# Optimization experiments

Measured on AMD Instinct MI355X. Metric: run time of the kernel, lower is better.

The kernel has to match this reference:

```python
import jax, jax.numpy as jnp
import numpy as np

Q_SIZE = 1024
K_SIZE = 1024
NUM_UNITS = 1024
B, T_Q, T_K = 16, 64, 128


def setup_inputs() -> dict:
    key = jax.random.key(0)
    k1, k2, k3, k4, k5 = jax.random.split(key, 5)
    stdv = 1.0 / np.sqrt(NUM_UNITS)
    query = jax.random.normal(k1, (B, T_Q, Q_SIZE), dtype=jnp.float32)
    keys = jax.random.normal(k2, (B, T_K, K_SIZE), dtype=jnp.float32)
    # nn.Linear(in, out, bias=False) weight has shape (out, in)
    Wq = jax.random.uniform(k3, (NUM_UNITS, Q_SIZE), dtype=jnp.float32,
                            minval=-stdv, maxval=stdv)
    Wk = jax.random.uniform(k4, (NUM_UNITS, K_SIZE), dtype=jnp.float32,
                            minval=-stdv, maxval=stdv)
    linear_att = jax.random.uniform(k5, (NUM_UNITS,), dtype=jnp.float32,
                                    minval=-stdv, maxval=stdv)
    normalize_scalar = jnp.full((1,), stdv, dtype=jnp.float32)
    normalize_bias = jnp.zeros((NUM_UNITS,), dtype=jnp.float32)
    return {"query": query, "keys": keys, "Wq": Wq, "Wk": Wk,
            "linear_att": linear_att, "normalize_scalar": normalize_scalar,
            "normalize_bias": normalize_bias}


def reference(query, keys, Wq, Wk, linear_att, normalize_scalar, normalize_bias):
    # batch_first=True, 3-d query, math='fp32', normalize=True, dropout=0, no mask
    att_query = jnp.einsum('bqi,ni->bqn', query, Wq)   # (b, t_q, n)
    att_keys = jnp.einsum('bki,ni->bkn', keys, Wk)     # (b, t_k, n)
    # broadcast sum + bias: (b, t_q, t_k, n)
    sum_qk = att_query[:, :, None, :] + att_keys[:, None, :, :] + normalize_bias
    la = linear_att / jnp.linalg.norm(linear_att)
    la = la * normalize_scalar  # (n,) via broadcast with (1,)
    scores = jnp.einsum('bqkn,n->bqk', jnp.tanh(sum_qk), la)  # (b, t_q, t_k)
    scores_normalized = jax.nn.softmax(scores, axis=-1)
    context = jnp.einsum('bqk,bkn->bqn', scores_normalized, keys)
    return context, scores_normalized
```

## Files before the change

kernel.cpp:

```cpp
#include <hip/hip_runtime.h>
#include <hip/hip_bf16.h>
#include <math.h>


#define ALPHA_2LOG2E 2.8853900817779268f
#define LOG2E 1.4426950408889634f

typedef __attribute__((ext_vector_type(8))) short short8;
typedef __attribute__((ext_vector_type(4))) float f32x4;
typedef __attribute__((ext_vector_type(2))) float f32x2;

static __device__ __forceinline__ short f2bf(float f) {
    union { float f; unsigned u; } v; v.f = f;
    unsigned r = v.u + 0x7fffu + ((v.u >> 16) & 1u);
    return (short)(r >> 16);
}

__global__ __launch_bounds__(256) void cast_prep_kernel(
    const float* __restrict__ q, const float* __restrict__ k,
    const float* __restrict__ wq, const float* __restrict__ wk,
    short* __restrict__ qb, short* __restrict__ kb,
    short* __restrict__ wqb, short* __restrict__ wkb,
    const float* __restrict__ la, const float* __restrict__ scal,
    float* __restrict__ la2, float* __restrict__ sla)
{
    const int bid = blockIdx.x;
    if (bid == 2560) {
        __shared__ float red[4];
        const int t = threadIdx.x, lane = t & 63, w = t >> 6;
        float ss = 0.f;
        for (int i = t; i < 1024; i += 256) { float v = la[i]; ss = fmaf(v, v, ss); }
        #pragma unroll
        for (int off = 32; off; off >>= 1) ss += __shfl_xor(ss, off, 64);
        if (lane == 0) red[w] = ss;
        __syncthreads();
        const float tot = red[0] + red[1] + red[2] + red[3];
        const float sc = scal[0] / sqrtf(tot);
        float s2 = 0.f;
        for (int i = t; i < 1024; i += 256) {
            float v = la[i] * sc;
            la2[i] = 2.f * v;
            s2 += v;
        }
        #pragma unroll
        for (int off = 32; off; off >>= 1) s2 += __shfl_xor(s2, off, 64);
        __syncthreads();
        if (lane == 0) red[w] = s2;
        __syncthreads();
        if (t == 0) sla[0] = red[0] + red[1] + red[2] + red[3];
        return;
    }
    const float* src; short* dst; int base;
    if (bid < 512)       { src = q;  dst = qb;  base = bid; }
    else if (bid < 1536) { src = k;  dst = kb;  base = bid - 512; }
    else if (bid < 2048) { src = wq; dst = wqb; base = bid - 1536; }
    else                 { src = wk; dst = wkb; base = bid - 2048; }
    const size_t i = ((size_t)base * 256 + threadIdx.x) * 8;
    float4 a = *reinterpret_cast<const float4*>(src + i);
    float4 b = *reinterpret_cast<const float4*>(src + i + 4);
    short8 o;
    o[0] = f2bf(a.x); o[1] = f2bf(a.y); o[2] = f2bf(a.z); o[3] = f2bf(a.w);
    o[4] = f2bf(b.x); o[5] = f2bf(b.y); o[6] = f2bf(b.z); o[7] = f2bf(b.w);
    *reinterpret_cast<short8*>(dst + i) = o;
}

__global__ __launch_bounds__(256) void gemm_mfma_kernel(
    const short* __restrict__ qb, const short* __restrict__ kb,
    const short* __restrict__ wqb, const short* __restrict__ wkb,
    const float* __restrict__ bias,
    float* __restrict__ aqE, float* __restrict__ akE)
{
    __shared__ short As[2][64][32];
    __shared__ short Bs[2][64][32];

    const int bid = blockIdx.x;
    const short* A; const short* W; float* C; int useBias, bm, bn, ldc;
    if (bid < 256) {
        A = qb;  W = wqb; C = aqE; useBias = 0; ldc = 1024;
        bm = (bid & 15) * 64; bn = (bid >> 4) * 64;
    } else {
        int b2 = bid - 256;
        A = wkb; W = kb;  C = akE; useBias = 1; ldc = 2048;
        bm = (b2 & 15) * 64; bn = (b2 >> 4) * 64;
    }

    const int t = threadIdx.x;
    const int lane = t & 63, wid = t >> 6;
    const int wr = wid >> 1, wc = wid & 1;
    const int fr = lane & 15, fg = lane >> 4;

    const int sRow = t >> 2, sSlot = t & 3;
    const short8* pA = (const short8*)(A + (size_t)bm * 1024);
    const short8* pB = (const short8*)(W + (size_t)bn * 1024);

    const f32x4 zero = {0.f, 0.f, 0.f, 0.f};
    f32x4 acc[2][2];
    acc[0][0] = zero; acc[0][1] = zero; acc[1][0] = zero; acc[1][1] = zero;

    short8 rA = pA[(size_t)sRow * 128 + sSlot];
    short8 rB = pB[(size_t)sRow * 128 + sSlot];
    *(short8*)&As[0][sRow][sSlot * 8] = rA;
    *(short8*)&Bs[0][sRow][sSlot * 8] = rB;
    rA = pA[(size_t)sRow * 128 + 4 + sSlot];
    rB = pB[(size_t)sRow * 128 + 4 + sSlot];
    asm volatile("s_waitcnt lgkmcnt(0)" ::: "memory");
    __builtin_amdgcn_s_barrier();
    asm volatile("" ::: "memory");

    #pragma unroll 1
    for (int kt = 0; kt < 32; ++kt) {
        const int cur = kt & 1;
        short8 af[2], bfr[2];
        #pragma unroll
        for (int mi = 0; mi < 2; ++mi)
            af[mi] = *(const short8*)&As[cur][wr * 32 + mi * 16 + fr][fg * 8];
        #pragma unroll
        for (int ni = 0; ni < 2; ++ni)
            bfr[ni] = *(const short8*)&Bs[cur][wc * 32 + ni * 16 + fr][fg * 8];
        if (kt < 31) {
            *(short8*)&As[cur ^ 1][sRow][sSlot * 8] = rA;
            *(short8*)&Bs[cur ^ 1][sRow][sSlot * 8] = rB;
        }
        if (kt < 30) {
            const int koff = (kt + 2) * 4 + sSlot;
            rA = pA[(size_t)sRow * 128 + koff];
            rB = pB[(size_t)sRow * 128 + koff];
        }
        #pragma unroll
        for (int mi = 0; mi < 2; ++mi)
            #pragma unroll
            for (int ni = 0; ni < 2; ++ni)
                acc[mi][ni] = __builtin_amdgcn_mfma_f32_16x16x32_bf16(
                    af[mi], bfr[ni], acc[mi][ni], 0, 0, 0);
        asm volatile("s_waitcnt lgkmcnt(0)" ::: "memory");
        __builtin_amdgcn_s_barrier();
        asm volatile("" ::: "memory");
    }

    float* Cb = C + (size_t)bm * ldc;
    #pragma unroll
    for (int mi = 0; mi < 2; ++mi) {
        const int row0 = wr * 32 + mi * 16 + fg * 4;
        float brow[4] = {0.f, 0.f, 0.f, 0.f};
        if (useBias) {
            #pragma unroll
            for (int r = 0; r < 4; ++r) brow[r] = bias[bm + row0 + r];
        }
        #pragma unroll
        for (int ni = 0; ni < 2; ++ni) {
            const int col = bn + wc * 32 + ni * 16 + fr;
            #pragma unroll
            for (int r = 0; r < 4; ++r)
                Cb[(size_t)(row0 + r) * ldc + col] =
                    __builtin_amdgcn_exp2f((acc[mi][ni][r] + brow[r]) * ALPHA_2LOG2E);
        }
    }
}

__global__ __launch_bounds__(1024) void scores_part_kernel(
    const float* __restrict__ aqE, const float* __restrict__ akE,
    const float* __restrict__ la2, float* __restrict__ partials)
{
    const int b = blockIdx.x, nc = blockIdx.y;
    const int t = threadIdx.x, w = t >> 6, lane = t & 63;

    __shared__ float eqs[64][64];
    __shared__ float eks[64][128];
    __shared__ float l2s[64];

    {
        const int qq = t >> 4, nj = (t & 15) << 2;
        *(float4*)&eqs[qq][nj] =
            *(const float4*)(aqE + ((size_t)((b << 6) + qq) << 10) + (nc << 6) + nj);
        const int n = t >> 4, k0 = (t & 15) << 3;
        const float* src = akE + ((size_t)((nc << 6) + n) << 11) + (b << 7) + k0;
        *(float4*)&eks[n][k0]     = *(const float4*)src;
        *(float4*)&eks[n][k0 + 4] = *(const float4*)(src + 4);
        if (t < 64) l2s[t] = la2[(nc << 6) + t];
    }
    __syncthreads();

    const int q0 = w << 2;
    f32x2 acc[4];
    #pragma unroll
    for (int i = 0; i < 4; ++i) acc[i] = (f32x2){0.f, 0.f};

    const int kb2 = lane << 1;
    #pragma unroll 4
    for (int np = 0; np < 32; ++np) {
        const int n0 = np << 1;
        const f32x2 ek0 = *(const f32x2*)&eks[n0][kb2];
        const f32x2 ek1 = *(const f32x2*)&eks[n0 + 1][kb2];
        const f32x2 l2 = *(const f32x2*)&l2s[n0];
        const float S = l2.x + l2.y;
        #pragma unroll
        for (int i = 0; i < 4; ++i) {
            const f32x2 eq = *(const f32x2*)&eqs[q0 + i][n0];
            const f32x2 E0 = eq.x * ek0;
            const f32x2 E1 = eq.y * ek1;
            const f32x2 d1 = E1 + 1.f;
            const f32x2 D  = E0 * d1 + d1;
            const f32x2 num = l2.x * E1 + (l2.y * E0 + S);
            f32x2 r;
            r.x = __builtin_amdgcn_rcpf(D.x);
            r.y = __builtin_amdgcn_rcpf(D.y);
            acc[i] = num * r + acc[i];
        }
    }

    float* pp = partials + ((size_t)((b << 4) + nc) << 13) + kb2;
    #pragma unroll
    for (int i = 0; i < 4; ++i)
        *(f32x2*)(pp + ((q0 + i) << 7)) = acc[i];
}

__global__ __launch_bounds__(256) void reduce_softmax_kernel(
    const float* __restrict__ partials, const float* __restrict__ sla,
    float* __restrict__ p_buf, float* __restrict__ out_scores)
{
    const int b = blockIdx.x, qo = blockIdx.y;
    const int t = threadIdx.x, w = t >> 6, lane = t & 63;
    const int q = (qo << 2) + w;

    const float* pp = partials + ((size_t)b << 17) + (q << 7) + (lane << 1);
    float s0 = 0.f, s1 = 0.f;
    #pragma unroll
    for (int nc = 0; nc < 16; ++nc) {
        const float2 v = *(const float2*)(pp + ((size_t)nc << 13));
        s0 += v.x; s1 += v.y;
    }
    const float Sla = sla[0];
    s0 = Sla - s0; s1 = Sla - s1;
    float m = fmaxf(s0, s1);
    #pragma unroll
    for (int off = 32; off; off >>= 1) m = fmaxf(m, __shfl_xor(m, off, 64));
    float e0 = __builtin_amdgcn_exp2f((s0 - m) * LOG2E);
    float e1 = __builtin_amdgcn_exp2f((s1 - m) * LOG2E);
    float s = e0 + e1;
    #pragma unroll
    for (int off = 32; off; off >>= 1) s += __shfl_xor(s, off, 64);
    const float inv = __builtin_amdgcn_rcpf(s);
    float2 p = {e0 * inv, e1 * inv};
    *(float2*)(p_buf + ((size_t)((b << 6) + q) << 7) + (lane << 1)) = p;
    *(float2*)(out_scores + ((size_t)((b << 6) + q) << 7) + (lane << 1)) = p;
}

__global__ __launch_bounds__(512) void ctx_kernel(
    const float* __restrict__ p_buf, const float* __restrict__ keys,
    float* __restrict__ ctx)
{
    const int b = blockIdx.x, nc = blockIdx.y;
    const int t = threadIdx.x;

    __shared__ float ks[128][64];
    __shared__ float ps[64][128];

    {
        const int k = t >> 2, n0 = (t & 3) << 4;
        const float* src = keys + ((size_t)((b << 7) + k) << 10) + (nc << 6) + n0;
        #pragma unroll
        for (int i = 0; i < 4; ++i)
            *(float4*)&ks[k][n0 + (i << 2)] = *(const float4*)(src + (i << 2));
        const int qq = t >> 3, k0 = (t & 7) << 4;
        const float* psrc = p_buf + ((size_t)((b << 6) + qq) << 7) + k0;
        #pragma unroll
        for (int i = 0; i < 4; ++i)
            *(float4*)&ps[qq][k0 + (i << 2)] = *(const float4*)(psrc + (i << 2));
    }
    __syncthreads();

    const int q0 = (t >> 5) << 2;
    const int n0 = (t & 31) << 1;
    float acc[4][2];
    #pragma unroll
    for (int i = 0; i < 4; ++i) { acc[i][0] = 0.f; acc[i][1] = 0.f; }

    #pragma unroll 8
    for (int k = 0; k < 128; ++k) {
        const float2 kv = *(const float2*)&ks[k][n0];
        #pragma unroll
        for (int i = 0; i < 4; ++i) {
            const float p = ps[q0 + i][k];
            acc[i][0] = fmaf(p, kv.x, acc[i][0]);
            acc[i][1] = fmaf(p, kv.y, acc[i][1]);
        }
    }
    #pragma unroll
    for (int i = 0; i < 4; ++i) {
        float2 v = {acc[i][0], acc[i][1]};
        *(float2*)(ctx + ((size_t)((b << 6) + q0 + i) << 10) + (nc << 6) + n0) = v;
    }
}

extern "C" void kernel_launch(void* const* d_in, const int* in_sizes, int n_in,
                              void* d_out, int out_size, void* d_ws, size_t ws_size,
                              hipStream_t stream) {
    const float* query  = (const float*)d_in[0];
    const float* keys   = (const float*)d_in[1];
    const float* Wq     = (const float*)d_in[2];
    const float* Wk     = (const float*)d_in[3];
    const float* la     = (const float*)d_in[4];
    const float* scal   = (const float*)d_in[5];
    const float* bias   = (const float*)d_in[6];

    float* ws  = (float*)d_ws;
    float* aqE = ws;
    float* akE = ws + (1u << 20);
    float* la2 = akE + (2u << 20);
    float* sla = la2 + 1024;
    short* qb  = (short*)(ws + 3 * 1048576 + 2048);
    short* kb  = qb + 1048576;
    short* wqb = kb + 2097152;
    short* wkb = wqb + 1048576;
    float* partials = (float*)kb;
    float* p_buf    = (float*)qb;

    float* ctx        = (float*)d_out;
    float* out_scores = ctx + (size_t)16 * 64 * 1024;

    cast_prep_kernel<<<2561, 256, 0, stream>>>(query, keys, Wq, Wk, qb, kb, wqb, wkb,
                                               la, scal, la2, sla);
    gemm_mfma_kernel<<<768, 256, 0, stream>>>(qb, kb, wqb, wkb, bias, aqE, akE);
    scores_part_kernel<<<dim3(16, 16), 1024, 0, stream>>>(aqE, akE, la2, partials);
    reduce_softmax_kernel<<<dim3(16, 16), 256, 0, stream>>>(partials, sla, p_buf, out_scores);
    ctx_kernel<<<dim3(16, 16), 512, 0, stream>>>(p_buf, keys, ctx);
}
```

Measured before the change: 59.99 us.

## Fuse softmax reduction into scores kernel via last-block counter; use direct-to-LDS loads in GEMM

Drops the separate reduce_softmax launch. The last of the 16 n-chunk blocks per batch, found with an atomic counter that cast_prep resets, sums the partials and computes the softmax itself. The GEMM's register-staged global-to-LDS copies are replaced with global_load_lds direct loads, issued one k-tile ahead. This saves a kernel launch and the register round-trip, but the per-batch softmax now runs serially in one block and relies on threadfence ordering.

```diff
diff --git a/kernel.cpp b/kernel.cpp
--- a/kernel.cpp
+++ b/kernel.cpp
@@ -14,6 +14,12 @@
     union { float f; unsigned u; } v; v.f = f;
     unsigned r = v.u + 0x7fffu + ((v.u >> 16) & 1u);
     return (short)(r >> 16);
+}
+
+static __device__ __forceinline__ void gload16(const void* g, void* l) {
+    __builtin_amdgcn_global_load_lds(
+        (const __attribute__((address_space(1))) unsigned*)g,
+        (__attribute__((address_space(3))) unsigned*)l, 16, 0, 0);
 }
 
 __global__ __launch_bounds__(256) void cast_prep_kernel(
@@ -22,12 +28,13 @@
     short* __restrict__ qb, short* __restrict__ kb,
     short* __restrict__ wqb, short* __restrict__ wkb,
     const float* __restrict__ la, const float* __restrict__ scal,
-    float* __restrict__ la2, float* __restrict__ sla)
+    float* __restrict__ la2, float* __restrict__ sla, int* __restrict__ cnt)
 {
     const int bid = blockIdx.x;
     if (bid == 2560) {
         __shared__ float red[4];
         const int t = threadIdx.x, lane = t & 63, w = t >> 6;
+        if (t < 16) cnt[t] = 0;
         float ss = 0.f;
         for (int i = t; i < 1024; i += 256) { float v = la[i]; ss = fmaf(v, v, ss); }
         #pragma unroll
@@ -89,27 +96,27 @@
     const int wr = wid >> 1, wc = wid & 1;
     const int fr = lane & 15, fg = lane >> 4;
 
-    const int sRow = t >> 2, sSlot = t & 3;
-    const short8* pA = (const short8*)(A + (size_t)bm * 1024);
-    const short8* pB = (const short8*)(W + (size_t)bn * 1024);
+    const short* gA0 = A + (size_t)(bm + (wid << 4) + (lane >> 2)) * 1024 + ((lane & 3) << 3);
+    const short* gB0 = W + (size_t)(bn + (wid << 4) + (lane >> 2)) * 1024 + ((lane & 3) << 3);
 
     const f32x4 zero = {0.f, 0.f, 0.f, 0.f};
     f32x4 acc[2][2];
     acc[0][0] = zero; acc[0][1] = zero; acc[1][0] = zero; acc[1][1] = zero;
 
-    short8 rA = pA[(size_t)sRow * 128 + sSlot];
-    short8 rB = pB[(size_t)sRow * 128 + sSlot];
-    *(short8*)&As[0][sRow][sSlot * 8] = rA;
-    *(short8*)&Bs[0][sRow][sSlot * 8] = rB;
-    rA = pA[(size_t)sRow * 128 + 4 + sSlot];
-    rB = pB[(size_t)sRow * 128 + 4 + sSlot];
-    asm volatile("s_waitcnt lgkmcnt(0)" ::: "memory");
+    gload16(gA0, &As[0][wid << 4][0]);
+    gload16(gB0, &Bs[0][wid << 4][0]);
+    asm volatile("s_waitcnt vmcnt(0)" ::: "memory");
     __builtin_amdgcn_s_barrier();
     asm volatile("" ::: "memory");
 
     #pragma unroll 1
     for (int kt = 0; kt < 32; ++kt) {
         const int cur = kt & 1;
+        if (kt < 31) {
+            const int ko = (kt + 1) << 5;
+            gload16(gA0 + ko, &As[cur ^ 1][wid << 4][0]);
+            gload16(gB0 + ko, &Bs[cur ^ 1][wid << 4][0]);
+        }
         short8 af[2], bfr[2];
         #pragma unroll
         for (int mi = 0; mi < 2; ++mi)
@@ -117,22 +124,13 @@
         #pragma unroll
         for (int ni = 0; ni < 2; ++ni)
             bfr[ni] = *(const short8*)&Bs[cur][wc * 32 + ni * 16 + fr][fg * 8];
-        if (kt < 31) {
-            *(short8*)&As[cur ^ 1][sRow][sSlot * 8] = rA;
-            *(short8*)&Bs[cur ^ 1][sRow][sSlot * 8] = rB;
-        }
-        if (kt < 30) {
-            const int koff = (kt + 2) * 4 + sSlot;
-            rA = pA[(size_t)sRow * 128 + koff];
-            rB = pB[(size_t)sRow * 128 + koff];
-        }
         #pragma unroll
         for (int mi = 0; mi < 2; ++mi)
             #pragma unroll
             for (int ni = 0; ni < 2; ++ni)
                 acc[mi][ni] = __builtin_amdgcn_mfma_f32_16x16x32_bf16(
                     af[mi], bfr[ni], acc[mi][ni], 0, 0, 0);
-        asm volatile("s_waitcnt lgkmcnt(0)" ::: "memory");
+        asm volatile("s_waitcnt vmcnt(0) lgkmcnt(0)" ::: "memory");
         __builtin_amdgcn_s_barrier();
         asm volatile("" ::: "memory");
     }
@@ -157,9 +155,11 @@
     }
 }
 
-__global__ __launch_bounds__(1024) void scores_part_kernel(
+__global__ __launch_bounds__(1024) void scores_kernel(
     const float* __restrict__ aqE, const float* __restrict__ akE,
-    const float* __restrict__ la2, float* __restrict__ partials)
+    const float* __restrict__ la2, const float* __restrict__ sla,
+    float* __restrict__ partials, float* __restrict__ p_buf,
+    float* __restrict__ out_scores, int* __restrict__ cnt)
 {
     const int b = blockIdx.x, nc = blockIdx.y;
     const int t = threadIdx.x, w = t >> 6, lane = t & 63;
@@ -167,6 +167,7 @@
     __shared__ float eqs[64][64];
     __shared__ float eks[64][128];
     __shared__ float l2s[64];
+    __shared__ int isLast;
 
     {
         const int qq = t >> 4, nj = (t & 15) << 2;
@@ -212,37 +213,39 @@
     #pragma unroll
     for (int i = 0; i < 4; ++i)
         *(f32x2*)(pp + ((q0 + i) << 7)) = acc[i];
-}
-
-__global__ __launch_bounds__(256) void reduce_softmax_kernel(
-    const float* __restrict__ partials, const float* __restrict__ sla,
-    float* __restrict__ p_buf, float* __restrict__ out_scores)
-{
-    const int b = blockIdx.x, qo = blockIdx.y;
-    const int t = threadIdx.x, w = t >> 6, lane = t & 63;
-    const int q = (qo << 2) + w;
-
-    const float* pp = partials + ((size_t)b << 17) + (q << 7) + (lane << 1);
-    float s0 = 0.f, s1 = 0.f;
-    #pragma unroll
-    for (int nc = 0; nc < 16; ++nc) {
-        const float2 v = *(const float2*)(pp + ((size_t)nc << 13));
-        s0 += v.x; s1 += v.y;
-    }
+
+    __threadfence();
+    __syncthreads();
+    if (t == 0) isLast = (atomicAdd(&cnt[b], 1) == 15);
+    __syncthreads();
+    if (!isLast) return;
+    __threadfence();
+
     const float Sla = sla[0];
-    s0 = Sla - s0; s1 = Sla - s1;
-    float m = fmaxf(s0, s1);
-    #pragma unroll
-    for (int off = 32; off; off >>= 1) m = fmaxf(m, __shfl_xor(m, off, 64));
-    float e0 = __builtin_amdgcn_exp2f((s0 - m) * LOG2E);
-    float e1 = __builtin_amdgcn_exp2f((s1 - m) * LOG2E);
-    float s = e0 + e1;
-    #pragma unroll
-    for (int off = 32; off; off >>= 1) s += __shfl_xor(s, off, 64);
-    const float inv = __builtin_amdgcn_rcpf(s);
-    float2 p = {e0 * inv, e1 * inv};
-    *(float2*)(p_buf + ((size_t)((b << 6) + q) << 7) + (lane << 1)) = p;
-    *(float2*)(out_scores + ((size_t)((b << 6) + q) << 7) + (lane << 1)) = p;
+    #pragma unroll
+    for (int qi = 0; qi < 4; ++qi) {
+        const int q = (w << 2) + qi;
+        const float* pq = partials + ((size_t)b << 17) + (q << 7) + kb2;
+        float s0 = 0.f, s1 = 0.f;
+        #pragma unroll
+        for (int c = 0; c < 16; ++c) {
+            const float2 v = *(const float2*)(pq + ((size_t)c << 13));
+            s0 += v.x; s1 += v.y;
+        }
+        s0 = Sla - s0; s1 = Sla - s1;
+        float m = fmaxf(s0, s1);
+        #pragma unroll
+        for (int off = 32; off; off >>= 1) m = fmaxf(m, __shfl_xor(m, off, 64));
+        float e0 = __builtin_amdgcn_exp2f((s0 - m) * LOG2E);
+        float e1 = __builtin_amdgcn_exp2f((s1 - m) * LOG2E);
+        float s = e0 + e1;
+        #pragma unroll
+        for (int off = 32; off; off >>= 1) s += __shfl_xor(s, off, 64);
+        const float inv = __builtin_amdgcn_rcpf(s);
+        float2 p = {e0 * inv, e1 * inv};
+        *(float2*)(p_buf + ((size_t)((b << 6) + q) << 7) + kb2) = p;
+        *(float2*)(out_scores + ((size_t)((b << 6) + q) << 7) + kb2) = p;
+    }
 }
 
 __global__ __launch_bounds__(512) void ctx_kernel(
@@ -308,6 +311,7 @@
     float* akE = ws + (1u << 20);
     float* la2 = akE + (2u << 20);
     float* sla = la2 + 1024;
+    int*   cnt = (int*)(sla + 1);
     short* qb  = (short*)(ws + 3 * 1048576 + 2048);
     short* kb  = qb + 1048576;
     short* wqb = kb + 2097152;
@@ -319,9 +323,9 @@
     float* out_scores = ctx + (size_t)16 * 64 * 1024;
 
     cast_prep_kernel<<<2561, 256, 0, stream>>>(query, keys, Wq, Wk, qb, kb, wqb, wkb,
-                                               la, scal, la2, sla);
+                                               la, scal, la2, sla, cnt);
     gemm_mfma_kernel<<<768, 256, 0, stream>>>(qb, kb, wqb, wkb, bias, aqE, akE);
-    scores_part_kernel<<<dim3(16, 16), 1024, 0, stream>>>(aqE, akE, la2, partials);
-    reduce_softmax_kernel<<<dim3(16, 16), 256, 0, stream>>>(partials, sla, p_buf, out_scores);
+    scores_kernel<<<dim3(16, 16), 1024, 0, stream>>>(aqE, akE, la2, sla,
+                                                     partials, p_buf, out_scores, cnt);
     ctx_kernel<<<dim3(16, 16), 512, 0, stream>>>(p_buf, keys, ctx);
 }
```

New measurement: 169.1 us. +181.8%, slower.
